# Optimization experiments

Hardware: AMD Instinct MI355X
Metric: run time of the kernel (lower is better)

The kernel has to match this reference:

```python
import jax, jax.numpy as jnp
import numpy as np

Q_MAX = 127.0  # 2^(8-1) - 1 for 8-bit activations


def _ste_round(x):
    # forward: round(x); backward: identity
    return x + jax.lax.stop_gradient(jnp.round(x) - x)


def setup_inputs() -> dict:
    key = jax.random.key(0)
    k1, k2 = jax.random.split(key)
    B, S, D_IN, D_OUT = 4, 4096, 2048, 2048
    x = jax.random.normal(k1, (B, S, D_IN), dtype=jnp.float32)
    # muP-style init: std = 1/sqrt(fan_in)
    weight = jax.random.normal(k2, (D_OUT, D_IN), dtype=jnp.float32) / np.sqrt(D_IN)
    return {"x": x, "weight": weight}


def reference(x, weight):
    # --- ternary weight quantization (AbsMean) ---
    w_scale = jnp.maximum(jnp.mean(jnp.abs(weight)), 1e-6)        # scalar
    w_norm = weight / w_scale
    w_quant = jnp.clip(_ste_round(w_norm), -1.0, 1.0)             # [O, I], values in {-1,0,1}

    # --- per-token absmax activation quantization (8-bit) ---
    a_scale = jnp.clip(jnp.max(jnp.abs(x), axis=-1, keepdims=True), 1e-8, None)  # [B,S,1]
    x_quant = jnp.clip(_ste_round(x * (Q_MAX / a_scale)), -Q_MAX, Q_MAX)         # [B,S,I]

    # --- scaled matmul: y = (x_q @ w_q^T) * w_scale * (a_scale / Q_MAX) ---
    y = jnp.einsum('bsi,oi->bso', x_quant, w_quant)
    y = y * (w_scale * (a_scale / Q_MAX))
    return y
```

## Files before the change

### kernel.cpp

```cpp
#include <hip/hip_runtime.h>
#include <hip/hip_bf16.h>

typedef int int4v __attribute__((ext_vector_type(4)));

#define K_DIM 2048
#define N_DIM 2048
#define M_DIM 16384
#define NW 4194304
#define BKB 128
#define NKT (K_DIM / BKB)

__device__ __forceinline__ char qi8(float v, double rr) {
  double q = rint((double)v * rr);
  q = fmin(fmax(q, -127.0), 127.0);
  return (char)(int)q;
}

__global__ void k_xquant(const float* __restrict__ x, float* __restrict__ ascale,
                         char* __restrict__ xq, const float4* __restrict__ w4,
                         double* __restrict__ red) {
  const int row = blockIdx.x;
  const int t = threadIdx.x;
  const float4* xr = (const float4*)(x + (size_t)row * K_DIM);
  float4 v0 = xr[t];
  float4 v1 = xr[t + 256];
  float m = fmaxf(fmaxf(fmaxf(fabsf(v0.x), fabsf(v0.y)), fmaxf(fabsf(v0.z), fabsf(v0.w))),
                  fmaxf(fmaxf(fabsf(v1.x), fabsf(v1.y)), fmaxf(fabsf(v1.z), fabsf(v1.w))));
  for (int o = 32; o; o >>= 1) m = fmaxf(m, __shfl_xor(m, o));
  __shared__ float sm[4];
  if ((t & 63) == 0) sm[t >> 6] = m;
  __syncthreads();
  float a = fmaxf(fmaxf(sm[0], sm[1]), fmaxf(sm[2], sm[3]));
  a = fmaxf(a, 1e-8f);
  if (t == 0) ascale[row] = a;
  double rr = 127.0 / (double)a;
  char4* qr4 = (char4*)(xq + (size_t)row * K_DIM);
  char4 a4, b4;
  a4.x = qi8(v0.x, rr); a4.y = qi8(v0.y, rr); a4.z = qi8(v0.z, rr); a4.w = qi8(v0.w, rr);
  b4.x = qi8(v1.x, rr); b4.y = qi8(v1.y, rr); b4.z = qi8(v1.z, rr); b4.w = qi8(v1.w, rr);
  qr4[t] = a4;
  qr4[t + 256] = b4;

  if (row < 256) {
    const int n4 = NW / 4;
    double s = 0.0;
    for (int i = row * 256 + t; i < n4; i += 256 * 256) {
      float4 v = w4[i];
      s += (double)fabsf(v.x) + (double)fabsf(v.y) + (double)fabsf(v.z) + (double)fabsf(v.w);
    }
    for (int o = 32; o; o >>= 1) s += __shfl_xor(s, o);
    __shared__ double sd[4];
    if ((t & 63) == 0) sd[t >> 6] = s;
    __syncthreads();
    if (t == 0) red[row] = (sd[0] + sd[1]) + (sd[2] + sd[3]);
  }
}

__device__ __forceinline__ char wq1(float v, double inv) {
  double r = rint((double)v * inv);
  r = fmin(fmax(r, -1.0), 1.0);
  return (char)(int)r;
}

__global__ void k_wquant(const float4* __restrict__ w4, const double* __restrict__ red,
                         double* __restrict__ wsd, char4* __restrict__ wq4) {
  __shared__ double sd[4];
  double s = red[threadIdx.x];
  for (int o = 32; o; o >>= 1) s += __shfl_xor(s, o);
  if ((threadIdx.x & 63) == 0) sd[threadIdx.x >> 6] = s;
  __syncthreads();
  double m = ((sd[0] + sd[1]) + (sd[2] + sd[3])) / (double)NW;
  double ws = (m > 1e-6) ? m : 1e-6;
  if (blockIdx.x == 0 && threadIdx.x == 0) *wsd = ws;
  double inv = 1.0 / ws;
  int i = blockIdx.x * blockDim.x + threadIdx.x;
  if (i >= NW / 4) return;
  float4 v = w4[i];
  char4 q;
  q.x = wq1(v.x, inv);
  q.y = wq1(v.y, inv);
  q.z = wq1(v.z, inv);
  q.w = wq1(v.w, inv);
  wq4[i] = q;
}

__device__ __forceinline__ void gload16(const void* g, void* l) {
  __builtin_amdgcn_global_load_lds(
      (const __attribute__((address_space(1))) void*)g,
      (__attribute__((address_space(3))) void*)l, 16, 0, 0);
}

#define RD_A(DST, CA, MH, CO)                                               \
  _Pragma("unroll") for (int mf = 0; mf < 4; ++mf)                          \
    DST[mf] = *(const int4v*)((CA) + (rA + (MH)*64 + mf * 16) * 128 + (CO));

#define RD_B(DST, CB, CO)                                                   \
  _Pragma("unroll") for (int nf = 0; nf < 4; ++nf)                          \
    DST[nf] = *(const int4v*)((CB) + (rB + nf * 16) * 128 + (CO));

#define MM(MH, AF, BF)                                                      \
  __builtin_amdgcn_s_setprio(1);                                            \
  _Pragma("unroll") for (int mf = 0; mf < 4; ++mf)                          \
  _Pragma("unroll") for (int nf = 0; nf < 4; ++nf)                          \
    acc[(MH)*4 + mf][nf] = __builtin_amdgcn_mfma_i32_16x16x64_i8(           \
        AF[mf], BF[nf], acc[(MH)*4 + mf][nf], 0, 0, 0);                     \
  __builtin_amdgcn_s_setprio(0);

#define KTILE(CB, NB, KT)                                                   \
  {                                                                         \
    const char* An = Ab + (((KT) + 1) & (NKT - 1)) * BKB;                   \
    const char* Bn = Bb + (((KT) + 1) & (NKT - 1)) * BKB;                   \
    _Pragma("unroll") for (int c = 0; c < 4; ++c)                           \
      gload16(An + soff[c], (NB) + loff[c]);                                \
    _Pragma("unroll") for (int c = 0; c < 4; ++c)                           \
      gload16(Bn + soff[c], (NB) + 32768 + loff[c]);                        \
    RD_A(aX, CB, 0, co0);                                                   \
    RD_B(bX, (CB) + 32768, co0);                                            \
    RD_A(aY, CB, 1, co0);                                                   \
    MM(0, aX, bX);                                                          \
    RD_B(bY, (CB) + 32768, co1);                                            \
    MM(1, aY, bX);                                                          \
    RD_A(aX, CB, 0, co1);                                                   \
    MM(0, aX, bY);                                                          \
    RD_A(aY, CB, 1, co1);                                                   \
    MM(1, aY, bY);                                                          \
    asm volatile("s_waitcnt vmcnt(0)" ::: "memory");                        \
    __builtin_amdgcn_s_barrier();                                           \
  }

__global__ __launch_bounds__(512, 1) void k_gemm(
    const char* __restrict__ xq, const char* __restrict__ wq,
    const float* __restrict__ ascale, const double* __restrict__ wsd,
    float* __restrict__ out) {
  __shared__ __align__(16) char lds[131072];
  char* buf0 = lds;
  char* buf1 = lds + 65536;

  const int tid = threadIdx.x;
  const int l = tid & 63;
  const int wv = tid >> 6;
  const int wm = wv >> 2;
  const int wn = wv & 3;
  const int g = l >> 4, r16 = l & 15;

  const int bid = blockIdx.x;
  const int logical = (bid & 7) * 64 + (bid >> 3);
  const int br = logical >> 3;
  const int bc = logical & 7;

  const char* Ab = xq + (size_t)br * 256 * K_DIM;
  const char* Bb = wq + (size_t)bc * 256 * K_DIM;

  int soff[4], loff[4];
#pragma unroll
  for (int c = 0; c < 4; ++c) {
    int lb = c * 8192 + tid * 16;
    loff[c] = lb;
    int row = lb >> 7;
    int cb = lb & 127;
    soff[c] = row * K_DIM + (cb ^ ((row & 7) << 4));
  }

  const int sw = (r16 & 7) << 4;
  const int co0 = (g * 16) ^ sw;
  const int co1 = (64 + g * 16) ^ sw;
  const int rA = wm * 128 + r16;
  const int rB = wn * 64 + r16;

  int4v acc[8][4];
#pragma unroll
  for (int mf = 0; mf < 8; ++mf)
#pragma unroll
    for (int nf = 0; nf < 4; ++nf) acc[mf][nf] = (int4v){0, 0, 0, 0};

#pragma unroll
  for (int c = 0; c < 4; ++c) gload16(Ab + soff[c], buf0 + loff[c]);
#pragma unroll
  for (int c = 0; c < 4; ++c) gload16(Bb + soff[c], buf0 + 32768 + loff[c]);
  asm volatile("s_waitcnt vmcnt(0)" ::: "memory");
  __builtin_amdgcn_s_barrier();

  int4v aX[4], aY[4], bX[4], bY[4];

  for (int kt = 0; kt < NKT; kt += 2) {
    KTILE(buf0, buf1, kt);
    KTILE(buf1, buf0, kt + 1);
  }

  float wsf = (float)(*wsd);
  size_t trow0 = (size_t)br * 256 + wm * 128;
  int oc0 = bc * 256 + wn * 64;
#pragma unroll
  for (int mf = 0; mf < 8; ++mf) {
#pragma unroll
    for (int j = 0; j < 4; ++j) {
      size_t t = trow0 + mf * 16 + g * 4 + j;
      float s = wsf * (ascale[t] / 127.0f);
      float* yr = out + t * (size_t)N_DIM + oc0;
#pragma unroll
      for (int nf = 0; nf < 4; ++nf) yr[nf * 16 + r16] = (float)acc[mf][nf][j] * s;
    }
  }
}

extern "C" void kernel_launch(void* const* d_in, const int* in_sizes, int n_in,
                              void* d_out, int out_size, void* d_ws, size_t ws_size,
                              hipStream_t stream) {
  const float* x = (const float*)d_in[0];
  const float* w = (const float*)d_in[1];
  float* out = (float*)d_out;

  char* ws = (char*)d_ws;
  double* red = (double*)ws;
  double* wsd = (double*)(ws + 2048);
  float* ascale = (float*)(ws + 4096);
  char* xq = (char*)(ws + 4096 + 65536);
  char* wq = xq + (size_t)M_DIM * K_DIM;

  k_xquant<<<M_DIM, 256, 0, stream>>>(x, ascale, xq, (const float4*)w, red);
  k_wquant<<<NW / 4 / 256, 256, 0, stream>>>((const float4*)w, red, wsd, (char4*)wq);
  k_gemm<<<dim3(N_DIM / 256 * M_DIM / 256), 512, 0, stream>>>(xq, wq, ascale, wsd, out);
}
```

Measured before the change: 115.6 us.

## Load GEMM B operand directly from global into double-buffered registers

The weight (B) tile no longer goes through LDS. Each wave loads its B fragments straight from global memory into registers, with a register double buffer that prefetches the next K tile. This halves LDS use, removes the B LDS reads and loosens the vmcnt wait to cover only the A loads. The cost is duplicated global/L2 traffic for B across waves that share the same wn, less coalesced 64-byte row segments, and more VGPRs held per wave.

```diff
diff --git a/kernel.cpp b/kernel.cpp
--- a/kernel.cpp
+++ b/kernel.cpp
@@ -94,10 +94,6 @@
   _Pragma("unroll") for (int mf = 0; mf < 4; ++mf)                          \
     DST[mf] = *(const int4v*)((CA) + (rA + (MH)*64 + mf * 16) * 128 + (CO));
 
-#define RD_B(DST, CB, CO)                                                   \
-  _Pragma("unroll") for (int nf = 0; nf < 4; ++nf)                          \
-    DST[nf] = *(const int4v*)((CB) + (rB + nf * 16) * 128 + (CO));
-
 #define MM(MH, AF, BF)                                                      \
   __builtin_amdgcn_s_setprio(1);                                            \
   _Pragma("unroll") for (int mf = 0; mf < 4; ++mf)                          \
@@ -106,25 +102,25 @@
         AF[mf], BF[nf], acc[(MH)*4 + mf][nf], 0, 0, 0);                     \
   __builtin_amdgcn_s_setprio(0);
 
-#define KTILE(CB, NB, KT)                                                   \
+#define KTILE(CB, NB, BC0, BC1, BN0, BN1, KT)                               \
   {                                                                         \
     const char* An = Ab + (((KT) + 1) & (NKT - 1)) * BKB;                   \
     const char* Bn = Bb + (((KT) + 1) & (NKT - 1)) * BKB;                   \
     _Pragma("unroll") for (int c = 0; c < 4; ++c)                           \
       gload16(An + soff[c], (NB) + loff[c]);                                \
-    _Pragma("unroll") for (int c = 0; c < 4; ++c)                           \
-      gload16(Bn + soff[c], (NB) + 32768 + loff[c]);                        \
+    _Pragma("unroll") for (int nf = 0; nf < 4; ++nf) {                      \
+      BN0[nf] = *(const int4v*)(Bn + sB[nf]);                               \
+      BN1[nf] = *(const int4v*)(Bn + sB[nf] + 64);                          \
+    }                                                                       \
     RD_A(aX, CB, 0, co0);                                                   \
-    RD_B(bX, (CB) + 32768, co0);                                            \
     RD_A(aY, CB, 1, co0);                                                   \
-    MM(0, aX, bX);                                                          \
-    RD_B(bY, (CB) + 32768, co1);                                            \
-    MM(1, aY, bX);                                                          \
+    MM(0, aX, BC0);                                                         \
+    MM(1, aY, BC0);                                                         \
     RD_A(aX, CB, 0, co1);                                                   \
-    MM(0, aX, bY);                                                          \
     RD_A(aY, CB, 1, co1);                                                   \
-    MM(1, aY, bY);                                                          \
-    asm volatile("s_waitcnt vmcnt(0)" ::: "memory");                        \
+    MM(0, aX, BC1);                                                         \
+    MM(1, aY, BC1);                                                         \
+    asm volatile("s_waitcnt vmcnt(8)" ::: "memory");                        \
     __builtin_amdgcn_s_barrier();                                           \
   }
 
@@ -132,9 +128,9 @@
     const char* __restrict__ xq, const char* __restrict__ wq,
     const float* __restrict__ ascale, const double* __restrict__ wsd,
     float* __restrict__ out) {
-  __shared__ __align__(16) char lds[131072];
+  __shared__ __align__(16) char lds[65536];
   char* buf0 = lds;
-  char* buf1 = lds + 65536;
+  char* buf1 = lds + 32768;
 
   const int tid = threadIdx.x;
   const int l = tid & 63;
@@ -165,7 +161,11 @@
   const int co0 = (g * 16) ^ sw;
   const int co1 = (64 + g * 16) ^ sw;
   const int rA = wm * 128 + r16;
-  const int rB = wn * 64 + r16;
+
+  int sB[4];
+#pragma unroll
+  for (int nf = 0; nf < 4; ++nf)
+    sB[nf] = (wn * 64 + nf * 16 + r16) * K_DIM + g * 16;
 
   int4v acc[8][4];
 #pragma unroll
@@ -175,16 +175,20 @@
 
 #pragma unroll
   for (int c = 0; c < 4; ++c) gload16(Ab + soff[c], buf0 + loff[c]);
-#pragma unroll
-  for (int c = 0; c < 4; ++c) gload16(Bb + soff[c], buf0 + 32768 + loff[c]);
-  asm volatile("s_waitcnt vmcnt(0)" ::: "memory");
+  int4v bc0[4], bc1[4], bn0[4], bn1[4];
+#pragma unroll
+  for (int nf = 0; nf < 4; ++nf) {
+    bc0[nf] = *(const int4v*)(Bb + sB[nf]);
+    bc1[nf] = *(const int4v*)(Bb + sB[nf] + 64);
+  }
+  asm volatile("s_waitcnt vmcnt(8)" ::: "memory");
   __builtin_amdgcn_s_barrier();
 
-  int4v aX[4], aY[4], bX[4], bY[4];
+  int4v aX[4], aY[4];
 
   for (int kt = 0; kt < NKT; kt += 2) {
-    KTILE(buf0, buf1, kt);
-    KTILE(buf1, buf0, kt + 1);
+    KTILE(buf0, buf1, bc0, bc1, bn0, bn1, kt);
+    KTILE(buf1, buf0, bn0, bn1, bc0, bc1, kt + 1);
   }
 
   float wsf = (float)(*wsd);
```

Result: slower. 155.5 us (+34.5%).
